# Kernel tuning notes

Measured on AMD Instinct MI355X. Metric: run time of the kernel, lower is better.

## Reference

```python
import jax, jax.numpy as jnp
import numpy as np

T, B, C = 1024, 16, 1024
H, K, PAD_L = 16, 7, 3  # num_heads, kernel_size, padding_l
OUT = 1024


def setup_inputs() -> dict:
    key = jax.random.key(0)
    ks = jax.random.split(key, 8)
    s_in = 1.0 / np.sqrt(C)
    return {
        "x": jax.random.normal(ks[0], (T, B, C), dtype=jnp.float32),
        "W1": jax.random.normal(ks[1], (C, C), dtype=jnp.float32) * s_in,
        "b1": jnp.zeros((C,), dtype=jnp.float32),
        "Wq": jax.random.normal(ks[2], (C, H * K), dtype=jnp.float32) * s_in,
        "bq": jnp.zeros((H * K,), dtype=jnp.float32),
        "conv_bias": jax.random.normal(ks[3], (C,), dtype=jnp.float32) * 0.02,
        "W2": jax.random.normal(ks[4], (C, OUT), dtype=jnp.float32) * s_in,
        "b2": jnp.zeros((OUT,), dtype=jnp.float32),
    }


def reference(x, W1, b1, Wq, bq, conv_bias, W2, b2):
    # linear1 (glu=False -> no activation)
    h = x @ W1 + b1                       # [T, B, C]
    Tn, Bn, Cn = h.shape
    R = Cn // H                           # channels per head
    # dynamic filter prediction from query (= h), softmax over K taps
    w = (h @ Wq + bq).reshape(Tn, Bn, H, K)
    w = jax.nn.softmax(w, axis=-1)        # [T, B, H, K]
    # unfold1d: pad PAD_L left, K-1-PAD_L right along time, gather K-windows
    hp = jnp.pad(h, ((PAD_L, K - 1 - PAD_L), (0, 0), (0, 0)))
    win = jnp.stack([hp[k:k + Tn] for k in range(K)], axis=-1)  # [T, B, C, K]
    win = win.reshape(Tn, Bn, H, R, K)
    out = jnp.einsum('tbhrk,tbhk->tbhr', win, w).reshape(Tn, Bn, Cn)
    out = out + conv_bias                 # [T, B, C]
    return out @ W2 + b2                  # [T, B, OUT]
```

## Files before the change

### kernel.cpp

```cpp
#include <hip/hip_runtime.h>
#include <math.h>

#define T_DIM 1024
#define B_DIM 16
#define C_DIM 1024
#define H_DIM 16
#define K_TAPS 7
#define PAD_LEFT 3
#define OUT_DIM 1024
#define M_DIM (T_DIM * B_DIM)
#define HK 112
#define HKP 128
#define KD 1024

typedef __attribute__((ext_vector_type(8))) short bf16x8;
typedef __attribute__((ext_vector_type(4))) float f32x4;

__device__ __forceinline__ ushort f2bf(float f) {
    union { float f; unsigned u; } v; v.f = f;
    unsigned u = v.u;
    u += 0x7fffu + ((u >> 16) & 1u);
    return (ushort)(u >> 16);
}
__device__ __forceinline__ float bf2f(ushort h) {
    union { unsigned u; float f; } v; v.u = ((unsigned)h) << 16;
    return v.f;
}

__global__ __launch_bounds__(256) void cvt_bf16x8(const float* __restrict__ in,
                                                  ushort* __restrict__ out,
                                                  int n8) {
    int i = blockIdx.x * blockDim.x + threadIdx.x;
    if (i >= n8) return;
    const float4* p = (const float4*)in;
    float4 a = p[2 * i], b = p[2 * i + 1];
    uint4 o;
    o.x = (unsigned)f2bf(a.x) | ((unsigned)f2bf(a.y) << 16);
    o.y = (unsigned)f2bf(a.z) | ((unsigned)f2bf(a.w) << 16);
    o.z = (unsigned)f2bf(b.x) | ((unsigned)f2bf(b.y) << 16);
    o.w = (unsigned)f2bf(b.z) | ((unsigned)f2bf(b.w) << 16);
    ((uint4*)out)[i] = o;
}

__global__ void transpose_all(const float* __restrict__ W1s,
                              const float* __restrict__ Wqs,
                              const float* __restrict__ W2s,
                              ushort* __restrict__ W1t,
                              ushort* __restrict__ Wqt,
                              ushort* __restrict__ W2t) {
    __shared__ float tile[32][33];
    int bx = blockIdx.x;
    const float* W; ushort* Wt; int N, Npad, nb;
    if (bx < 32)      { W = W1s; Wt = W1t; N = 1024; Npad = 1024; nb = bx; }
    else if (bx < 36) { W = Wqs; Wt = Wqt; N = 112;  Npad = 128;  nb = bx - 32; }
    else              { W = W2s; Wt = W2t; N = 1024; Npad = 1024; nb = bx - 36; }
    int n0 = nb * 32, k0 = blockIdx.y * 32;
    int tx = threadIdx.x, ty = threadIdx.y;
#pragma unroll
    for (int j = 0; j < 4; ++j) {
        int k = k0 + ty * 4 + j;
        int n = n0 + tx;
        tile[ty * 4 + j][tx] = (n < N) ? W[(size_t)k * N + n] : 0.f;
    }
    __syncthreads();
#pragma unroll
    for (int j = 0; j < 4; ++j) {
        int n = n0 + ty * 4 + j;
        if (n < Npad)
            Wt[(size_t)n * KD + k0 + tx] = f2bf(tile[tx][ty * 4 + j]);
    }
}

#define PHASE(P2KS, MH, READB, STAGE_STMT, VM_STMT)                           \
    {                                                                         \
        if (READB) {                                                          \
            _Pragma("unroll")                                                 \
            for (int n = 0; n < 4; ++n)                                       \
                b[n] = *(const bf16x8*)(Bbase + (P2KS)*8192 + bOff + n*512);  \
        }                                                                     \
        bf16x8 a_[4];                                                         \
        _Pragma("unroll")                                                     \
        for (int m = 0; m < 4; ++m)                                           \
            a_[m] = *(const bf16x8*)(Abase + (P2KS)*8192 + aOff +             \
                                     (MH)*2048 + m*512);                      \
        STAGE_STMT;                                                           \
        VM_STMT;                                                              \
        __builtin_amdgcn_s_barrier();                                         \
        asm volatile("s_waitcnt lgkmcnt(0)" ::: "memory");                    \
        __builtin_amdgcn_sched_barrier(0);                                    \
        __builtin_amdgcn_s_setprio(1);                                        \
        _Pragma("unroll")                                                     \
        for (int m = 0; m < 4; ++m)                                           \
            _Pragma("unroll")                                                 \
            for (int n = 0; n < 4; ++n)                                       \
                acc[(MH)*4 + m][n] = __builtin_amdgcn_mfma_f32_16x16x32_bf16( \
                    a_[m], b[n], acc[(MH)*4 + m][n], 0, 0, 0);                \
        __builtin_amdgcn_s_setprio(0);                                        \
        __builtin_amdgcn_s_barrier();                                         \
        __builtin_amdgcn_sched_barrier(0);                                    \
    }

template <bool OUT_BF16>
__global__ __launch_bounds__(512, 1) void gemm8p(
    const ushort* __restrict__ A, const ushort* __restrict__ Bt,
    const float* __restrict__ bias, void* __restrict__ Cp, int ldc) {
    __shared__ ushort Lds[8 * 8192];

    const int tid  = threadIdx.x;
    const int lane = tid & 63;
    const int wid  = tid >> 6;
    const int wr = wid >> 2;
    const int wc = wid & 3;
    const int fr = lane & 15;
    const int fq = lane >> 4;

    const int orig = blockIdx.x;
    const int nid  = (orig & 7) * 32 + (orig >> 3);
    const int bm = (nid >> 2) * 256;
    const int bn = (nid & 3) * 256;

    const int srow = tid >> 2;
    const int scol = ((tid & 3) ^ ((tid >> 3) & 3)) * 8;
    const size_t sA = (size_t)(bm + srow) * KD + scol;
    const size_t sB = (size_t)(bn + srow) * KD + scol;
    const int sdst = wid * 64 * 8;

    const int slotSw = (fq ^ ((fr >> 1) & 3)) * 8;
    const int aOff = (wr * 128 + fr) * 32 + slotSw;
    const int bOff = (wc * 64 + fr) * 32 + slotSw;
    const ushort* Abase = &Lds[0];
    const ushort* Bbase = &Lds[4 * 8192];

    f32x4 acc[8][4];
#pragma unroll
    for (int m = 0; m < 8; ++m)
#pragma unroll
        for (int n = 0; n < 4; ++n) acc[m][n] = (f32x4){0.f, 0.f, 0.f, 0.f};

    auto stageA = [&](int slot, int koff) {
#pragma unroll
        for (int i = 0; i < 2; ++i)
            __builtin_amdgcn_global_load_lds(
                (const __attribute__((address_space(1))) void*)(A + sA + koff + (size_t)i * 128 * KD),
                (__attribute__((address_space(3))) void*)(&Lds[slot * 8192 + i * 4096 + sdst]),
                16, 0, 0);
    };
    auto stageB = [&](int slot, int koff) {
#pragma unroll
        for (int i = 0; i < 2; ++i)
            __builtin_amdgcn_global_load_lds(
                (const __attribute__((address_space(1))) void*)(Bt + sB + koff + (size_t)i * 128 * KD),
                (__attribute__((address_space(3))) void*)(&Lds[(4 + slot) * 8192 + i * 4096 + sdst]),
                16, 0, 0);
    };

    stageA(0, 0);   stageB(0, 0);
    stageA(1, 32);  stageB(1, 32);
    stageA(2, 64);  stageB(2, 64);
    stageA(3, 96);  stageB(3, 96);
    asm volatile("s_waitcnt vmcnt(12)" ::: "memory");
    __builtin_amdgcn_sched_barrier(0);
    __builtin_amdgcn_s_barrier();
    __builtin_amdgcn_sched_barrier(0);

#pragma unroll 1
    for (int j = 0; j < 8; ++j) {
        bf16x8 b[4];
        const int e = 2 * j;

        PHASE(0, 0, 1,
              { if (j >= 1) stageA(3, (e + 1) * 64 + 32); },
              { asm volatile("s_waitcnt vmcnt(6)" ::: "memory");
                __builtin_amdgcn_sched_barrier(0); })
        PHASE(0, 1, 0,
              { if (j >= 1) stageB(3, (e + 1) * 64 + 32); },
              (void)0; )
        PHASE(1, 0, 1,
              { if (j < 7) stageA(0, (e + 2) * 64); },
              { if (j == 7) { asm volatile("s_waitcnt vmcnt(4)" ::: "memory"); }
                else        { asm volatile("s_waitcnt vmcnt(6)" ::: "memory"); }
                __builtin_amdgcn_sched_barrier(0); })
        PHASE(1, 1, 0,
              { if (j < 7) stageB(0, (e + 2) * 64); },
              (void)0; )
        PHASE(2, 0, 1,
              { if (j < 7) stageA(1, (e + 2) * 64 + 32); },
              { if (j == 7) { asm volatile("s_waitcnt vmcnt(0)" ::: "memory"); }
                else        { asm volatile("s_waitcnt vmcnt(6)" ::: "memory"); }
                __builtin_amdgcn_sched_barrier(0); })
        PHASE(2, 1, 0,
              { if (j < 7) stageB(1, (e + 2) * 64 + 32); },
              (void)0; )
        PHASE(3, 0, 1,
              { if (j < 7) stageA(2, (e + 3) * 64); },
              { asm volatile("s_waitcnt vmcnt(6)" ::: "memory");
                __builtin_amdgcn_sched_barrier(0); })
        PHASE(3, 1, 0,
              { if (j < 7) stageB(2, (e + 3) * 64); },
              (void)0; )
    }

#pragma unroll
    for (int n = 0; n < 4; ++n) {
        int col = bn + wc * 64 + n * 16 + fr;
        float bv = bias[col];
#pragma unroll
        for (int m = 0; m < 8; ++m) {
#pragma unroll
            for (int r = 0; r < 4; ++r) {
                int row = bm + wr * 128 + m * 16 + fq * 4 + r;
                float v = acc[m][n][r] + bv;
                if (OUT_BF16)
                    ((ushort*)Cp)[(size_t)row * ldc + col] = f2bf(v);
                else
                    ((float*)Cp)[(size_t)row * ldc + col] = v;
            }
        }
    }
}

__global__ __launch_bounds__(256) void gemm_small(const ushort* __restrict__ A,
                                                  const ushort* __restrict__ Bt,
                                                  const float* __restrict__ bias,
                                                  float* __restrict__ Cp) {
    __shared__ ushort Als[64 * 32];
    __shared__ ushort Bls[128 * 32];
    const int tid  = threadIdx.x;
    const int lane = tid & 63;
    const int wid  = tid >> 6;
    const int wr = wid >> 1, wc = wid & 1;
    const int bm = blockIdx.y * 64;
    const int fq = lane >> 4, fr = lane & 15;

    f32x4 acc[2][4];
#pragma unroll
    for (int m = 0; m < 2; ++m)
#pragma unroll
        for (int n = 0; n < 4; ++n) acc[m][n] = (f32x4){0.f, 0.f, 0.f, 0.f};

    const int rA = tid >> 2, oA = (tid & 3) * 8;
    for (int k0 = 0; k0 < KD; k0 += 32) {
        __builtin_amdgcn_global_load_lds(
            (const __attribute__((address_space(1))) void*)&A[(size_t)(bm + rA) * KD + k0 + oA],
            (__attribute__((address_space(3))) void*)&Als[wid * 64 * 8], 16, 0, 0);
#pragma unroll
        for (int i = 0; i < 2; ++i) {
            int c = i * 256 + tid;
            __builtin_amdgcn_global_load_lds(
                (const __attribute__((address_space(1))) void*)&Bt[(size_t)(c >> 2) * KD + k0 + (c & 3) * 8],
                (__attribute__((address_space(3))) void*)&Bls[(i * 256 + wid * 64) * 8], 16, 0, 0);
        }
        __syncthreads();

        bf16x8 af[2], bfr[4];
#pragma unroll
        for (int m = 0; m < 2; ++m)
            af[m] = *(const bf16x8*)&Als[(wr * 32 + m * 16 + fr) * 32 + fq * 8];
#pragma unroll
        for (int n = 0; n < 4; ++n)
            bfr[n] = *(const bf16x8*)&Bls[(wc * 64 + n * 16 + fr) * 32 + fq * 8];
#pragma unroll
        for (int m = 0; m < 2; ++m)
#pragma unroll
            for (int n = 0; n < 4; ++n)
                acc[m][n] = __builtin_amdgcn_mfma_f32_16x16x32_bf16(
                    af[m], bfr[n], acc[m][n], 0, 0, 0);
        __syncthreads();
    }

#pragma unroll
    for (int m = 0; m < 2; ++m) {
#pragma unroll
        for (int n = 0; n < 4; ++n) {
            int col = wc * 64 + n * 16 + fr;
            if (col >= HK) continue;
            float bv = bias[col];
#pragma unroll
            for (int r = 0; r < 4; ++r) {
                int row = bm + wr * 32 + m * 16 + fq * 4 + r;
                Cp[(size_t)row * HK + col] = acc[m][n][r] + bv;
            }
        }
    }
}

__global__ __launch_bounds__(256) void dynconv2(const ushort* __restrict__ h,
                                                const float* __restrict__ q,
                                                const float* __restrict__ cbias,
                                                ushort* __restrict__ out) {
    __shared__ ushort hw[22][1024];
    __shared__ float wsm[16][HK];
    const int tid = threadIdx.x;
    const int b  = blockIdx.x & 15;
    const int t0 = (blockIdx.x >> 4) << 4;

    for (int i = tid; i < 22 * 128; i += 256) {
        int wrow = i >> 7;
        int c8   = (i & 127) * 8;
        int tt   = t0 + wrow - PAD_LEFT;
        uint4 v = make_uint4(0, 0, 0, 0);
        if (tt >= 0 && tt < T_DIM)
            v = *(const uint4*)&h[((size_t)tt * B_DIM + b) * C_DIM + c8];
        *(uint4*)&hw[wrow][c8] = v;
    }
    {
        int tl = tid >> 4, hh = tid & 15;
        int m = (t0 + tl) * B_DIM + b;
        const float* p = &q[(size_t)m * HK + hh * K_TAPS];
        float mx = p[0];
#pragma unroll
        for (int k = 1; k < K_TAPS; ++k) mx = fmaxf(mx, p[k]);
        float e[K_TAPS], s = 0.f;
#pragma unroll
        for (int k = 0; k < K_TAPS; ++k) { e[k] = __expf(p[k] - mx); s += e[k]; }
        float inv = 1.f / s;
#pragma unroll
        for (int k = 0; k < K_TAPS; ++k) wsm[tl][hh * K_TAPS + k] = e[k] * inv;
    }
    __syncthreads();

    const int c  = tid * 4;
    const int hh = c >> 6;
    float4 bias = *(const float4*)&cbias[c];

    for (int tl = 0; tl < 16; ++tl) {
        float a0 = bias.x, a1 = bias.y, a2 = bias.z, a3 = bias.w;
#pragma unroll
        for (int k = 0; k < K_TAPS; ++k) {
            ushort4 hv = *(const ushort4*)&hw[tl + k][c];
            float wk = wsm[tl][hh * K_TAPS + k];
            a0 = fmaf(bf2f(hv.x), wk, a0);
            a1 = fmaf(bf2f(hv.y), wk, a1);
            a2 = fmaf(bf2f(hv.z), wk, a2);
            a3 = fmaf(bf2f(hv.w), wk, a3);
        }
        ushort4 o;
        o.x = f2bf(a0); o.y = f2bf(a1); o.z = f2bf(a2); o.w = f2bf(a3);
        *(ushort4*)&out[((size_t)(t0 + tl) * B_DIM + b) * C_DIM + c] = o;
    }
}

extern "C" void kernel_launch(void* const* d_in, const int* in_sizes, int n_in,
                              void* d_out, int out_size, void* d_ws,
                              size_t ws_size, hipStream_t stream) {
    const float* x     = (const float*)d_in[0];
    const float* W1    = (const float*)d_in[1];
    const float* b1    = (const float*)d_in[2];
    const float* Wq    = (const float*)d_in[3];
    const float* bq    = (const float*)d_in[4];
    const float* cbias = (const float*)d_in[5];
    const float* W2    = (const float*)d_in[6];
    const float* b2    = (const float*)d_in[7];
    float* out = (float*)d_out;

    ushort* xb    = (ushort*)d_ws;
    ushort* hb    = xb    + (size_t)M_DIM * C_DIM;
    ushort* convb = hb    + (size_t)M_DIM * C_DIM;
    ushort* W1t   = convb + (size_t)M_DIM * C_DIM;
    ushort* W2t   = W1t   + (size_t)C_DIM * C_DIM;
    ushort* Wqt   = W2t   + (size_t)C_DIM * OUT_DIM;
    float*  q     = (float*)(Wqt + (size_t)HKP * C_DIM);

    cvt_bf16x8<<<dim3(M_DIM * C_DIM / 8 / 256), dim3(256), 0, stream>>>(
        x, xb, M_DIM * C_DIM / 8);
    transpose_all<<<dim3(68, 32), dim3(32, 8), 0, stream>>>(
        W1, Wq, W2, W1t, Wqt, W2t);

    gemm8p<true><<<dim3(256), dim3(512), 0, stream>>>(xb, W1t, b1, hb, C_DIM);

    gemm_small<<<dim3(1, M_DIM / 64), dim3(256), 0, stream>>>(hb, Wqt, bq, q);

    dynconv2<<<dim3(B_DIM * T_DIM / 16), dim3(256), 0, stream>>>(
        hb, q, cbias, convb);

    gemm8p<false><<<dim3(256), dim3(512), 0, stream>>>(convb, W2t, b2, out,
                                                       OUT_DIM);
}
```

Baseline: 150.3 us.

## Replace 8-wave GEMM with 4-wave triple-buffered register-prefetch pipeline

The two large GEMMs now use a 256x128 tile with 4 waves and 512 blocks instead of a 256x256 tile with 8 waves and 256 blocks. A three-slot LDS ring keeps loads in flight three K-steps ahead, and the next step's fragments are double-buffered in registers so LDS reads overlap the current MFMAs, with one barrier per K-step. The aim is to cut barrier and LDS-wait stalls and raise the block count for better CU coverage. In exchange, more registers are held per wave and each block reuses less data, since every tile of A is now loaded twice.

```diff
diff --git a/kernel.cpp b/kernel.cpp
--- a/kernel.cpp
+++ b/kernel.cpp
@@ -12,6 +12,7 @@
 #define HK 112
 #define HKP 128
 #define KD 1024
+#define NTP 32
 
 typedef __attribute__((ext_vector_type(8))) short bf16x8;
 typedef __attribute__((ext_vector_type(4))) float f32x4;
@@ -71,65 +72,86 @@
     }
 }
 
-#define PHASE(P2KS, MH, READB, STAGE_STMT, VM_STMT)                           \
+#define STAGE_T(BUFI, T)                                                      \
     {                                                                         \
-        if (READB) {                                                          \
+        const ushort* Ap = A + srcA0 + (T) * 32;                              \
+        const ushort* Bp = Bt + srcB0 + (T) * 32;                             \
+        _Pragma("unroll")                                                     \
+        for (int i = 0; i < 4; ++i)                                           \
+            __builtin_amdgcn_global_load_lds(                                 \
+                (const __attribute__((address_space(1))) void*)(Ap + (size_t)i * 64 * KD), \
+                (__attribute__((address_space(3))) void*)(&Abuf[BUFI][(i * 256 + wid * 64) * 8]), \
+                16, 0, 0);                                                    \
+        _Pragma("unroll")                                                     \
+        for (int i = 0; i < 2; ++i)                                           \
+            __builtin_amdgcn_global_load_lds(                                 \
+                (const __attribute__((address_space(1))) void*)(Bp + (size_t)i * 64 * KD), \
+                (__attribute__((address_space(3))) void*)(&Bbuf[BUFI][(i * 256 + wid * 64) * 8]), \
+                16, 0, 0);                                                    \
+    }
+
+#define GITER(T, CA, CB, NA, NB)                                              \
+    {                                                                         \
+        if ((T) < NTP - 2) {                                                  \
+            asm volatile("s_waitcnt vmcnt(6)" ::: "memory");                  \
+        } else {                                                              \
+            asm volatile("s_waitcnt vmcnt(0)" ::: "memory");                  \
+        }                                                                     \
+        __builtin_amdgcn_sched_barrier(0);                                    \
+        __builtin_amdgcn_s_barrier();                                         \
+        __builtin_amdgcn_sched_barrier(0);                                    \
+        if ((T) < NTP - 3) STAGE_T((T) % 3, (T) + 3)                          \
+        if ((T) < NTP - 1) {                                                  \
+            const ushort* Ar = &Abuf[((T) + 1) % 3][0];                       \
+            const ushort* Br = &Bbuf[((T) + 1) % 3][0];                       \
+            _Pragma("unroll")                                                 \
+            for (int m = 0; m < 8; ++m)                                       \
+                NA[m] = *(const bf16x8*)(Ar + aBase + m * 512);               \
             _Pragma("unroll")                                                 \
             for (int n = 0; n < 4; ++n)                                       \
-                b[n] = *(const bf16x8*)(Bbase + (P2KS)*8192 + bOff + n*512);  \
+                NB[n] = *(const bf16x8*)(Br + bBase + n * 512);               \
         }                                                                     \
-        bf16x8 a_[4];                                                         \
-        _Pragma("unroll")                                                     \
-        for (int m = 0; m < 4; ++m)                                           \
-            a_[m] = *(const bf16x8*)(Abase + (P2KS)*8192 + aOff +             \
-                                     (MH)*2048 + m*512);                      \
-        STAGE_STMT;                                                           \
-        VM_STMT;                                                              \
-        __builtin_amdgcn_s_barrier();                                         \
-        asm volatile("s_waitcnt lgkmcnt(0)" ::: "memory");                    \
         __builtin_amdgcn_sched_barrier(0);                                    \
         __builtin_amdgcn_s_setprio(1);                                        \
         _Pragma("unroll")                                                     \
-        for (int m = 0; m < 4; ++m)                                           \
+        for (int m = 0; m < 8; ++m)                                           \
             _Pragma("unroll")                                                 \
             for (int n = 0; n < 4; ++n)                                       \
-                acc[(MH)*4 + m][n] = __builtin_amdgcn_mfma_f32_16x16x32_bf16( \
-                    a_[m], b[n], acc[(MH)*4 + m][n], 0, 0, 0);                \
+                acc[m][n] = __builtin_amdgcn_mfma_f32_16x16x32_bf16(          \
+                    CA[m], CB[n], acc[m][n], 0, 0, 0);                        \
         __builtin_amdgcn_s_setprio(0);                                        \
-        __builtin_amdgcn_s_barrier();                                         \
+        asm volatile("s_waitcnt lgkmcnt(0)" ::: "memory");                    \
         __builtin_amdgcn_sched_barrier(0);                                    \
     }
 
 template <bool OUT_BF16>
-__global__ __launch_bounds__(512, 1) void gemm8p(
+__global__ __launch_bounds__(256, 1) void gemm_pipe(
     const ushort* __restrict__ A, const ushort* __restrict__ Bt,
     const float* __restrict__ bias, void* __restrict__ Cp, int ldc) {
-    __shared__ ushort Lds[8 * 8192];
+    __shared__ ushort Abuf[3][256 * 32];
+    __shared__ ushort Bbuf[3][128 * 32];
 
     const int tid  = threadIdx.x;
     const int lane = tid & 63;
     const int wid  = tid >> 6;
-    const int wr = wid >> 2;
-    const int wc = wid & 3;
+    const int wr = wid >> 1;
+    const int wc = wid & 1;
     const int fr = lane & 15;
     const int fq = lane >> 4;
 
     const int orig = blockIdx.x;
-    const int nid  = (orig & 7) * 32 + (orig >> 3);
-    const int bm = (nid >> 2) * 256;
-    const int bn = (nid & 3) * 256;
-
-    const int srow = tid >> 2;
-    const int scol = ((tid & 3) ^ ((tid >> 3) & 3)) * 8;
-    const size_t sA = (size_t)(bm + srow) * KD + scol;
-    const size_t sB = (size_t)(bn + srow) * KD + scol;
-    const int sdst = wid * 64 * 8;
+    const int nid  = (orig & 7) * 64 + (orig >> 3);
+    const int bm = (nid >> 3) * 256;
+    const int bn = (nid & 7) * 128;
+
+    const int rA    = tid >> 2;
+    const int colSw = ((tid & 3) ^ ((tid >> 3) & 3)) * 8;
+    const size_t srcA0 = (size_t)(bm + rA) * KD + colSw;
+    const size_t srcB0 = (size_t)(bn + rA) * KD + colSw;
 
     const int slotSw = (fq ^ ((fr >> 1) & 3)) * 8;
-    const int aOff = (wr * 128 + fr) * 32 + slotSw;
-    const int bOff = (wc * 64 + fr) * 32 + slotSw;
-    const ushort* Abase = &Lds[0];
-    const ushort* Bbase = &Lds[4 * 8192];
+    const int aBase = (wr * 128 + fr) * 32 + slotSw;
+    const int bBase = (wc * 64 + fr) * 32 + slotSw;
 
     f32x4 acc[8][4];
 #pragma unroll
@@ -137,67 +159,32 @@
 #pragma unroll
         for (int n = 0; n < 4; ++n) acc[m][n] = (f32x4){0.f, 0.f, 0.f, 0.f};
 
-    auto stageA = [&](int slot, int koff) {
-#pragma unroll
-        for (int i = 0; i < 2; ++i)
-            __builtin_amdgcn_global_load_lds(
-                (const __attribute__((address_space(1))) void*)(A + sA + koff + (size_t)i * 128 * KD),
-                (__attribute__((address_space(3))) void*)(&Lds[slot * 8192 + i * 4096 + sdst]),
-                16, 0, 0);
-    };
-    auto stageB = [&](int slot, int koff) {
-#pragma unroll
-        for (int i = 0; i < 2; ++i)
-            __builtin_amdgcn_global_load_lds(
-                (const __attribute__((address_space(1))) void*)(Bt + sB + koff + (size_t)i * 128 * KD),
-                (__attribute__((address_space(3))) void*)(&Lds[(4 + slot) * 8192 + i * 4096 + sdst]),
-                16, 0, 0);
-    };
-
-    stageA(0, 0);   stageB(0, 0);
-    stageA(1, 32);  stageB(1, 32);
-    stageA(2, 64);  stageB(2, 64);
-    stageA(3, 96);  stageB(3, 96);
+    bf16x8 fAa[8], fAb[4], fBa[8], fBb[4];
+
+    STAGE_T(0, 0)
+    STAGE_T(1, 1)
+    STAGE_T(2, 2)
     asm volatile("s_waitcnt vmcnt(12)" ::: "memory");
     __builtin_amdgcn_sched_barrier(0);
     __builtin_amdgcn_s_barrier();
     __builtin_amdgcn_sched_barrier(0);
+    {
+        const ushort* Ar = &Abuf[0][0];
+        const ushort* Br = &Bbuf[0][0];
+#pragma unroll
+        for (int m = 0; m < 8; ++m)
+            fAa[m] = *(const bf16x8*)(Ar + aBase + m * 512);
+#pragma unroll
+        for (int n = 0; n < 4; ++n)
+            fAb[n] = *(const bf16x8*)(Br + bBase + n * 512);
+    }
+    asm volatile("s_waitcnt lgkmcnt(0)" ::: "memory");
+    __builtin_amdgcn_sched_barrier(0);
 
 #pragma unroll 1
-    for (int j = 0; j < 8; ++j) {
-        bf16x8 b[4];
-        const int e = 2 * j;
-
-        PHASE(0, 0, 1,
-              { if (j >= 1) stageA(3, (e + 1) * 64 + 32); },
-              { asm volatile("s_waitcnt vmcnt(6)" ::: "memory");
-                __builtin_amdgcn_sched_barrier(0); })
-        PHASE(0, 1, 0,
-              { if (j >= 1) stageB(3, (e + 1) * 64 + 32); },
-              (void)0; )
-        PHASE(1, 0, 1,
-              { if (j < 7) stageA(0, (e + 2) * 64); },
-              { if (j == 7) { asm volatile("s_waitcnt vmcnt(4)" ::: "memory"); }
-                else        { asm volatile("s_waitcnt vmcnt(6)" ::: "memory"); }
-                __builtin_amdgcn_sched_barrier(0); })
-        PHASE(1, 1, 0,
-              { if (j < 7) stageB(0, (e + 2) * 64); },
-              (void)0; )
-        PHASE(2, 0, 1,
-              { if (j < 7) stageA(1, (e + 2) * 64 + 32); },
-              { if (j == 7) { asm volatile("s_waitcnt vmcnt(0)" ::: "memory"); }
-                else        { asm volatile("s_waitcnt vmcnt(6)" ::: "memory"); }
-                __builtin_amdgcn_sched_barrier(0); })
-        PHASE(2, 1, 0,
-              { if (j < 7) stageB(1, (e + 2) * 64 + 32); },
-              (void)0; )
-        PHASE(3, 0, 1,
-              { if (j < 7) stageA(2, (e + 3) * 64); },
-              { asm volatile("s_waitcnt vmcnt(6)" ::: "memory");
-                __builtin_amdgcn_sched_barrier(0); })
-        PHASE(3, 1, 0,
-              { if (j < 7) stageB(2, (e + 3) * 64); },
-              (void)0; )
+    for (int t = 0; t < NTP; t += 2) {
+        GITER(t,     fAa, fAb, fBa, fBb)
+        GITER(t + 1, fBa, fBb, fAa, fAb)
     }
 
 #pragma unroll
@@ -366,13 +353,14 @@
     transpose_all<<<dim3(68, 32), dim3(32, 8), 0, stream>>>(
         W1, Wq, W2, W1t, Wqt, W2t);
 
-    gemm8p<true><<<dim3(256), dim3(512), 0, stream>>>(xb, W1t, b1, hb, C_DIM);
+    gemm_pipe<true><<<dim3(512), dim3(256), 0, stream>>>(xb, W1t, b1, hb,
+                                                         C_DIM);
 
     gemm_small<<<dim3(1, M_DIM / 64), dim3(256), 0, stream>>>(hb, Wqt, bq, q);
 
     dynconv2<<<dim3(B_DIM * T_DIM / 16), dim3(256), 0, stream>>>(
         hb, q, cbias, convb);
 
-    gemm8p<false><<<dim3(256), dim3(512), 0, stream>>>(convb, W2t, b2, out,
-                                                       OUT_DIM);
-}
+    gemm_pipe<false><<<dim3(512), dim3(256), 0, stream>>>(convb, W2t, b2, out,
+                                                          OUT_DIM);
+}
```

New measurement: 202.4 us. +34.7%, slower.
